# Optimization experiments

Measured on AMD Instinct MI355X. Metric: run time of the kernel, lower is better.

Reference implementation:

```python
import jax, jax.numpy as jnp
import numpy as np

# dims
B, N, K, V = 1, 50000, 6, 4          # batch, surface points, neighbors (num_sample_points-1), variables
P = K + 1                             # total sample points per node (center + K neighbors)
D_GEO, D_POS = 128, 32                # geometry / positional encoding widths
N_PARAMS, D_PARAM = 2, 32             # global params and their encoding width
D_IN = 7                              # 3 coords + 3 normals + 1 log-area
H1, H2 = 256, 128                     # MLP hidden widths
D_AGG = H1 + D_POS + D_GEO + D_PARAM  # aggregation-model input width = 448


def setup_inputs() -> dict:
    key = jax.random.key(0)
    ks = jax.random.split(key, 18)
    nrm = lambda k, s: jax.random.normal(k, s, jnp.float32)
    uni = lambda k, s, lo, hi: jax.random.uniform(k, s, jnp.float32, lo, hi)
    return {
        "surface_mesh_centers": nrm(ks[0], (B, N, 3)),
        "encoding_g": nrm(ks[1], (B, N, D_GEO)),
        "encoding_node": nrm(ks[2], (B, N, D_POS)),
        "surface_mesh_neighbors": nrm(ks[3], (B, N, K, 3)),
        "surface_normals": nrm(ks[4], (B, N, 3)),
        "surface_neighbors_normals": nrm(ks[5], (B, N, K, 3)),
        "surface_areas": uni(ks[6], (B, N, 1), 0.01, 1.0),
        "surface_neighbors_areas": uni(ks[7], (B, N, K, 1), 0.01, 1.0),
        "global_params_values": uni(ks[8], (B, N_PARAMS, 1), 0.5, 2.0),
        "global_params_reference": uni(ks[9], (B, N_PARAMS, 1), 0.5, 2.0),
        # learned parameters (per-variable MLPs stacked on leading V axis)
        "param_W": nrm(ks[10], (N_PARAMS, D_PARAM)) * 0.1,
        "param_b": jnp.zeros((D_PARAM,), jnp.float32),
        "basis_W1": nrm(ks[11], (V, D_IN, H1)) * 0.1,
        "basis_b1": jnp.zeros((V, H1), jnp.float32),
        "basis_W2": nrm(ks[12], (V, H1, H1)) * 0.1,
        "basis_b2": jnp.zeros((V, H1), jnp.float32),
        "agg_W1": nrm(ks[13], (V, D_AGG, H1)) * 0.1,
        "agg_b1": jnp.zeros((V, H1), jnp.float32),
        "agg_W2": nrm(ks[14], (V, H1, H2)) * 0.1,
        "agg_b2": jnp.zeros((V, H2), jnp.float32),
        "agg_W3": nrm(ks[15], (V, H2, 1)) * 0.1,
        "agg_b3": jnp.zeros((V, 1), jnp.float32),
    }


def reference(surface_mesh_centers, encoding_g, encoding_node, surface_mesh_neighbors,
              surface_normals, surface_neighbors_normals, surface_areas,
              surface_neighbors_areas, global_params_values, global_params_reference,
              param_W, param_b, basis_W1, basis_b1, basis_W2, basis_b2,
              agg_W1, agg_b1, agg_W2, agg_b2, agg_W3, agg_b3):
    relu = jax.nn.relu

    # parameter encoding: normalize globals by reference, broadcast to points, small MLP
    p = (global_params_values / global_params_reference)[:, :, 0]       # (B, n_params)
    p = jnp.broadcast_to(p[:, None, :], (B, N, N_PARAMS))               # (B, N, n_params)
    param_enc = relu(p @ param_W + param_b)                             # (B, N, D_PARAM)

    # concat coords + normals + log(area)/10, exactly as the torch module
    centers = jnp.concatenate(
        [surface_mesh_centers, surface_normals, jnp.log(surface_areas) / 10.0], -1)          # (B,N,7)
    neighbors = jnp.concatenate(
        [surface_mesh_neighbors, surface_neighbors_normals,
         jnp.log(surface_neighbors_areas) / 10.0], -1)                                        # (B,N,K,7)

    nb = neighbors + 1e-6
    vol = jnp.concatenate([centers[:, :, None, :], nb], axis=2)          # (B,N,P,7); p=0 is center
    # 1/dist computed in the 7-dim concatenated feature space (matches torch code)
    inv_dist = 1.0 / jnp.linalg.norm(centers[:, :, None, :] - nb, axis=-1, keepdims=True)    # (B,N,K,1)
    dist_sum = inv_dist.sum(axis=2)                                      # (B,N,1)

    ctx = jnp.concatenate([encoding_node, encoding_g, param_enc], -1)    # (B,N,Dctx)
    ctx = jnp.broadcast_to(ctx[:, :, None, :], (B, N, P, ctx.shape[-1]))

    outs = []
    for v in range(V):  # small fixed loop over output variables
        h = relu(vol @ basis_W1[v] + basis_b1[v])                        # (B,N,P,H1)
        basis = relu(h @ basis_W2[v] + basis_b2[v])                      # (B,N,P,H1)
        a = jnp.concatenate([basis, ctx], -1)                            # (B,N,P,D_AGG)
        a = relu(a @ agg_W1[v] + agg_b1[v])
        a = relu(a @ agg_W2[v] + agg_b2[v])
        a = a @ agg_W3[v] + agg_b3[v]                                    # (B,N,P,1)
        out_center = a[:, :, 0]                                          # (B,N,1)
        out_neighbor = (a[:, :, 1:] * inv_dist).sum(axis=2)              # (B,N,1)
        outs.append(0.5 * out_center + 0.5 * out_neighbor / dist_sum)
    return jnp.concatenate(outs, axis=-1)                                # (B,N,V)
```

## Files before the change

kernel.cpp:

```cpp
#include <hip/hip_runtime.h>

typedef __attribute__((ext_vector_type(8))) _Float16 f16x8;
typedef __attribute__((ext_vector_type(4))) float f32x4;

namespace {
constexpr int N_PTS = 50000;
constexpr int VOUT  = 4;
constexpr int PPB   = 9;
constexpr int MROWS = 64;
constexpr int ABYTES = 896;

constexpr int OFF_BW1 = 0;
constexpr int OFF_BW2 = 32768;
constexpr int OFF_AW1 = 294912;
constexpr int OFF_AW2 = 753664;
constexpr int PACK_TOTAL = 884736;
}

__global__ __launch_bounds__(256) void pack_weights_kernel(
    const float* __restrict__ bW1, const float* __restrict__ bW2,
    const float* __restrict__ aW1, const float* __restrict__ aW2,
    _Float16* __restrict__ out) {
  int t = blockIdx.x * 256 + threadIdx.x;
  const float* W; int Kg, N, Ksrc, base;
  if (t < OFF_BW2)      { base = OFF_BW1; Kg = 4;  N = 256; Ksrc = 7;   W = bW1; }
  else if (t < OFF_AW1) { base = OFF_BW2; Kg = 32; N = 256; Ksrc = 256; W = bW2; }
  else if (t < OFF_AW2) { base = OFF_AW1; Kg = 56; N = 256; Ksrc = 448; W = aW1; }
  else                  { base = OFF_AW2; Kg = 32; N = 128; Ksrc = 256; W = aW2; }
  int local = t - base;
  int vsz = Kg * N * 8;
  int v = local / vsz;
  int rem = local - v * vsz;
  int g  = rem / (N * 8);
  int r2 = rem - g * (N * 8);
  int n = r2 >> 3;
  int j = r2 & 7;
  int k = g * 8 + j;
  float val = (k < Ksrc) ? W[(v * Ksrc + k) * N + n] : 0.0f;
  out[t] = (_Float16)val;
}

template<int NT>
__device__ __forceinline__ void run_gemm(
    const _Float16* __restrict__ Bp, int Nn, int KB,
    const char* __restrict__ Ab, int abytes, int aswz,
    int lane, int n0, f32x4 acc[4][NT]) {
  const int q = lane >> 4, c = lane & 15;
  const char* Bb = (const char*)Bp;
  f16x8 bcur[NT], bnext[NT];
#pragma unroll
  for (int nt = 0; nt < NT; nt++)
    bcur[nt] = *(const f16x8*)(Bb + ((q * Nn + n0 + 16 * nt + c) << 4));
  for (int kb = 0; kb < KB; kb++) {
    f16x8 a[4];
    const int koff = (kb * 64 + q * 16) ^ aswz;
#pragma unroll
    for (int mt = 0; mt < 4; mt++)
      a[mt] = *(const f16x8*)(Ab + (16 * mt + c) * abytes + koff);
    if (kb + 1 < KB) {
#pragma unroll
      for (int nt = 0; nt < NT; nt++)
        bnext[nt] = *(const f16x8*)(Bb + ((((kb + 1) * 4 + q) * Nn + n0 + 16 * nt + c) << 4));
    }
#pragma unroll
    for (int mt = 0; mt < 4; mt++)
#pragma unroll
      for (int nt = 0; nt < NT; nt++)
        acc[mt][nt] = __builtin_amdgcn_mfma_f32_16x16x32_f16(a[mt], bcur[nt], acc[mt][nt], 0, 0, 0);
    if (kb + 1 < KB) {
#pragma unroll
      for (int nt = 0; nt < NT; nt++) bcur[nt] = bnext[nt];
    }
  }
}

template<int NT>
__device__ __forceinline__ void epilogue_relu(
    f32x4 acc[4][NT], const float* __restrict__ bias,
    int lane, int n0, char* __restrict__ Ab) {
  const int q = lane >> 4, c = lane & 15;
#pragma unroll
  for (int nt = 0; nt < NT; nt++) {
    const int col = n0 + 16 * nt + c;
    const float bv = bias[col];
#pragma unroll
    for (int mt = 0; mt < 4; mt++) {
#pragma unroll
      for (int r = 0; r < 4; r++) {
        const int row = 16 * mt + 4 * q + r;
        float y = fmaxf(acc[mt][nt][r] + bv, 0.0f);
        *(_Float16*)(Ab + row * ABYTES + ((2 * col) ^ (((4 * q + r) & 7) << 4))) = (_Float16)y;
      }
    }
  }
}

__global__ __launch_bounds__(256, 2) void surf_mfma_kernel(
    const float* __restrict__ centers, const float* __restrict__ enc_g,
    const float* __restrict__ enc_node, const float* __restrict__ nbrs,
    const float* __restrict__ normals, const float* __restrict__ nbr_normals,
    const float* __restrict__ areas, const float* __restrict__ nbr_areas,
    const float* __restrict__ gpv, const float* __restrict__ gpr,
    const float* __restrict__ pW, const float* __restrict__ pb,
    const float* __restrict__ bb1, const float* __restrict__ bb2,
    const float* __restrict__ ab1, const float* __restrict__ ab2,
    const float* __restrict__ aW3, const float* __restrict__ ab3,
    const _Float16* __restrict__ Wp, float* __restrict__ out) {
  __shared__ _Float16 sA[MROWS * 448];
  __shared__ _Float16 sVol[MROWS * 40];
  __shared__ float sVolF[63][7];
  __shared__ float sPE[32];
  __shared__ float sW3[128];
  __shared__ float sPart[4][64];
  __shared__ float sRow[64];
  __shared__ float sInvd[54];

  const int t    = threadIdx.x;
  const int lane = t & 63;
  const int w    = t >> 6;
  const int blk  = blockIdx.x;
  char* Ab = (char*)sA;

  if (t < 32) {
    float q0 = gpv[0] / gpr[0], q1 = gpv[1] / gpr[1];
    sPE[t] = fmaxf(fmaf(q0, pW[t], fmaf(q1, pW[32 + t], pb[t])), 0.0f);
  }
  if (t < 64) {
    float f[7];
    if (t < 63) {
      int pt = t / 7, p = t - pt * 7;
      int n = min(blk * PPB + pt, N_PTS - 1);
      if (p == 0) {
        f[0] = centers[n * 3];     f[1] = centers[n * 3 + 1]; f[2] = centers[n * 3 + 2];
        f[3] = normals[n * 3];     f[4] = normals[n * 3 + 1]; f[5] = normals[n * 3 + 2];
        f[6] = logf(areas[n]) * 0.1f;
      } else {
        int k = p - 1;
        int b3i = (n * 6 + k) * 3;
        f[0] = nbrs[b3i] + 1e-6f;        f[1] = nbrs[b3i + 1] + 1e-6f;
        f[2] = nbrs[b3i + 2] + 1e-6f;    f[3] = nbr_normals[b3i] + 1e-6f;
        f[4] = nbr_normals[b3i + 1] + 1e-6f; f[5] = nbr_normals[b3i + 2] + 1e-6f;
        f[6] = logf(nbr_areas[n * 6 + k]) * 0.1f + 1e-6f;
      }
#pragma unroll
      for (int j = 0; j < 7; j++) sVolF[t][j] = f[j];
    } else {
#pragma unroll
      for (int j = 0; j < 7; j++) f[j] = 0.0f;
    }
#pragma unroll
    for (int j = 0; j < 7; j++) sVol[t * 40 + j] = (_Float16)f[j];
#pragma unroll
    for (int j = 7; j < 40; j++) sVol[t * 40 + j] = (_Float16)0.0f;
  }
  __syncthreads();

  if (t < 54) {
    int pt = t / 6, k = t - pt * 6;
    float ss = 0.0f;
#pragma unroll
    for (int j = 0; j < 7; j++) {
      float d = sVolF[pt * 7][j] - sVolF[pt * 7 + 1 + k][j];
      ss = fmaf(d, d, ss);
    }
    sInvd[t] = 1.0f / sqrtf(ss);
  }
  for (int idx = t; idx < 63 * 192; idx += 256) {
    int row = idx / 192, j = idx - row * 192;
    int n = min(blk * PPB + row / 7, N_PTS - 1);
    float val = (j < 32) ? enc_node[n * 32 + j]
              : (j < 160) ? enc_g[n * 128 + (j - 32)]
              : sPE[j - 160];
    *(_Float16*)(Ab + row * ABYTES + ((2 * (256 + j)) ^ ((row & 7) << 4))) = (_Float16)val;
  }
  __syncthreads();

  const int aswz = (lane & 7) << 4;
  const int n0w  = 64 * w;

  for (int v = 0; v < VOUT; v++) {
    {
      f32x4 acc[4][4] = {};
      run_gemm<4>(Wp + OFF_BW1 + v * 8192, 256, 1, (const char*)sVol, 80, 0, lane, n0w, acc);
      epilogue_relu<4>(acc, bb1 + v * 256, lane, n0w, Ab);
    }
    __syncthreads();
    {
      f32x4 acc[4][4] = {};
      run_gemm<4>(Wp + OFF_BW2 + v * 65536, 256, 8, Ab, ABYTES, aswz, lane, n0w, acc);
      __syncthreads();
      epilogue_relu<4>(acc, bb2 + v * 256, lane, n0w, Ab);
    }
    __syncthreads();
    {
      f32x4 acc[4][4] = {};
      run_gemm<4>(Wp + OFF_AW1 + v * 114688, 256, 14, Ab, ABYTES, aswz, lane, n0w, acc);
      __syncthreads();
      epilogue_relu<4>(acc, ab1 + v * 256, lane, n0w, Ab);
    }
    __syncthreads();
    {
      f32x4 acc[4][2] = {};
      run_gemm<2>(Wp + OFF_AW2 + v * 32768, 128, 8, Ab, ABYTES, aswz, lane, 32 * w, acc);
      __syncthreads();
      epilogue_relu<2>(acc, ab2 + v * 128, lane, 32 * w, Ab);
      if (t < 128) sW3[t] = aW3[v * 128 + t];
    }
    __syncthreads();
    {
      int row = t & 63, h = t >> 6;
      float s = 0.0f;
      int swzm = (row & 7) << 4;
#pragma unroll
      for (int cc = 0; cc < 4; cc++) {
        int k0 = h * 32 + cc * 8;
        f16x8 av = *(const f16x8*)(Ab + row * ABYTES + ((2 * k0) ^ swzm));
#pragma unroll
        for (int j = 0; j < 8; j++) s = fmaf((float)av[j], sW3[k0 + j], s);
      }
      sPart[h][row] = s;
    }
    __syncthreads();
    if (t < 64) sRow[t] = sPart[0][t] + sPart[1][t] + sPart[2][t] + sPart[3][t] + ab3[v];
    __syncthreads();
    if (t < PPB) {
      int n = blk * PPB + t;
      if (n < N_PTS) {
        float o0 = sRow[t * 7];
        float on = 0.0f, ds = 0.0f;
#pragma unroll
        for (int k = 0; k < 6; k++) {
          float id = sInvd[t * 6 + k];
          on = fmaf(sRow[t * 7 + 1 + k], id, on);
          ds += id;
        }
        out[n * VOUT + v] = 0.5f * o0 + 0.5f * on / ds;
      }
    }
    __syncthreads();
  }
}

extern "C" void kernel_launch(void* const* d_in, const int* in_sizes, int n_in,
                              void* d_out, int out_size, void* d_ws, size_t ws_size,
                              hipStream_t stream) {
  const float* centers     = (const float*)d_in[0];
  const float* enc_g       = (const float*)d_in[1];
  const float* enc_node    = (const float*)d_in[2];
  const float* nbrs        = (const float*)d_in[3];
  const float* normals     = (const float*)d_in[4];
  const float* nbr_normals = (const float*)d_in[5];
  const float* areas       = (const float*)d_in[6];
  const float* nbr_areas   = (const float*)d_in[7];
  const float* gpv         = (const float*)d_in[8];
  const float* gpr         = (const float*)d_in[9];
  const float* pW          = (const float*)d_in[10];
  const float* pb          = (const float*)d_in[11];
  const float* bW1         = (const float*)d_in[12];
  const float* bb1         = (const float*)d_in[13];
  const float* bW2         = (const float*)d_in[14];
  const float* bb2         = (const float*)d_in[15];
  const float* aW1         = (const float*)d_in[16];
  const float* ab1         = (const float*)d_in[17];
  const float* aW2         = (const float*)d_in[18];
  const float* ab2         = (const float*)d_in[19];
  const float* aW3         = (const float*)d_in[20];
  const float* ab3         = (const float*)d_in[21];
  float* out = (float*)d_out;
  _Float16* Wp = (_Float16*)d_ws;

  pack_weights_kernel<<<dim3(PACK_TOTAL / 256), dim3(256), 0, stream>>>(
      bW1, bW2, aW1, aW2, Wp);

  const int nblocks = (N_PTS + PPB - 1) / PPB;
  surf_mfma_kernel<<<dim3(nblocks), dim3(256), 0, stream>>>(
      centers, enc_g, enc_node, nbrs, normals, nbr_normals, areas, nbr_areas,
      gpv, gpr, pW, pb, bb1, bb2, ab1, ab2, aW3, ab3, Wp, out);
}
```

Baseline: 744.8 us.

## Use 512-thread blocks, narrow per-wave tiles, fuse last layer into epilogue

Doubles the block to 8 waves, so each wave computes half as many output columns per GEMM. This halves the accumulator registers per thread and lets the launch bounds ask for more resident waves, to hide weight-load and LDS latency. The final 128→1 layer is folded into the AW2 GEMM epilogue with wave shuffles, dropping a separate LDS pass and two barriers. The context fill now loads float4s and writes packed 8×f16 vectors. The tighter launch bounds (512, 4) risk register spills, and LDS usage may still cap how many blocks stay resident.

```diff
diff --git a/kernel.cpp b/kernel.cpp
--- a/kernel.cpp
+++ b/kernel.cpp
@@ -7,7 +7,6 @@
 constexpr int N_PTS = 50000;
 constexpr int VOUT  = 4;
 constexpr int PPB   = 9;
-constexpr int MROWS = 64;
 constexpr int ABYTES = 896;
 
 constexpr int OFF_BW1 = 0;
@@ -95,7 +94,7 @@
   }
 }
 
-__global__ __launch_bounds__(256, 2) void surf_mfma_kernel(
+__global__ __launch_bounds__(512, 4) void surf_mfma_kernel(
     const float* __restrict__ centers, const float* __restrict__ enc_g,
     const float* __restrict__ enc_node, const float* __restrict__ nbrs,
     const float* __restrict__ normals, const float* __restrict__ nbr_normals,
@@ -106,12 +105,11 @@
     const float* __restrict__ ab1, const float* __restrict__ ab2,
     const float* __restrict__ aW3, const float* __restrict__ ab3,
     const _Float16* __restrict__ Wp, float* __restrict__ out) {
-  __shared__ _Float16 sA[MROWS * 448];
-  __shared__ _Float16 sVol[MROWS * 40];
+  __shared__ _Float16 sA[64 * 448];
+  __shared__ _Float16 sVol[64 * 40];
   __shared__ float sVolF[63][7];
-  __shared__ float sPE[32];
-  __shared__ float sW3[128];
-  __shared__ float sPart[4][64];
+  __shared__ alignas(16) float sPE[32];
+  __shared__ float sPart[8][64];
   __shared__ float sRow[64];
   __shared__ float sInvd[54];
 
@@ -165,64 +163,88 @@
     }
     sInvd[t] = 1.0f / sqrtf(ss);
   }
-  for (int idx = t; idx < 63 * 192; idx += 256) {
-    int row = idx / 192, j = idx - row * 192;
+  for (int task = t; task < 63 * 24; task += 512) {
+    int row = task / 24, g = task - row * 24;
     int n = min(blk * PPB + row / 7, N_PTS - 1);
-    float val = (j < 32) ? enc_node[n * 32 + j]
-              : (j < 160) ? enc_g[n * 128 + (j - 32)]
-              : sPE[j - 160];
-    *(_Float16*)(Ab + row * ABYTES + ((2 * (256 + j)) ^ ((row & 7) << 4))) = (_Float16)val;
+    float4 lo, hi;
+    if (g < 4) {
+      lo = *(const float4*)(enc_node + n * 32 + g * 8);
+      hi = *(const float4*)(enc_node + n * 32 + g * 8 + 4);
+    } else if (g < 20) {
+      lo = *(const float4*)(enc_g + n * 128 + (g - 4) * 8);
+      hi = *(const float4*)(enc_g + n * 128 + (g - 4) * 8 + 4);
+    } else {
+      lo = *(const float4*)(sPE + (g - 20) * 8);
+      hi = *(const float4*)(sPE + (g - 20) * 8 + 4);
+    }
+    f16x8 pk;
+    pk[0] = (_Float16)lo.x; pk[1] = (_Float16)lo.y; pk[2] = (_Float16)lo.z; pk[3] = (_Float16)lo.w;
+    pk[4] = (_Float16)hi.x; pk[5] = (_Float16)hi.y; pk[6] = (_Float16)hi.z; pk[7] = (_Float16)hi.w;
+    *(f16x8*)(Ab + row * ABYTES + ((512 + 16 * g) ^ ((row & 7) << 4))) = pk;
   }
   __syncthreads();
 
   const int aswz = (lane & 7) << 4;
-  const int n0w  = 64 * w;
+  const int n0w  = 32 * w;
 
   for (int v = 0; v < VOUT; v++) {
     {
-      f32x4 acc[4][4] = {};
-      run_gemm<4>(Wp + OFF_BW1 + v * 8192, 256, 1, (const char*)sVol, 80, 0, lane, n0w, acc);
-      epilogue_relu<4>(acc, bb1 + v * 256, lane, n0w, Ab);
-    }
-    __syncthreads();
-    {
-      f32x4 acc[4][4] = {};
-      run_gemm<4>(Wp + OFF_BW2 + v * 65536, 256, 8, Ab, ABYTES, aswz, lane, n0w, acc);
-      __syncthreads();
-      epilogue_relu<4>(acc, bb2 + v * 256, lane, n0w, Ab);
-    }
-    __syncthreads();
-    {
-      f32x4 acc[4][4] = {};
-      run_gemm<4>(Wp + OFF_AW1 + v * 114688, 256, 14, Ab, ABYTES, aswz, lane, n0w, acc);
-      __syncthreads();
-      epilogue_relu<4>(acc, ab1 + v * 256, lane, n0w, Ab);
+      f32x4 acc[4][2] = {};
+      run_gemm<2>(Wp + OFF_BW1 + v * 8192, 256, 1, (const char*)sVol, 80, 0, lane, n0w, acc);
+      epilogue_relu<2>(acc, bb1 + v * 256, lane, n0w, Ab);
     }
     __syncthreads();
     {
       f32x4 acc[4][2] = {};
-      run_gemm<2>(Wp + OFF_AW2 + v * 32768, 128, 8, Ab, ABYTES, aswz, lane, 32 * w, acc);
+      run_gemm<2>(Wp + OFF_BW2 + v * 65536, 256, 8, Ab, ABYTES, aswz, lane, n0w, acc);
       __syncthreads();
-      epilogue_relu<2>(acc, ab2 + v * 128, lane, 32 * w, Ab);
-      if (t < 128) sW3[t] = aW3[v * 128 + t];
+      epilogue_relu<2>(acc, bb2 + v * 256, lane, n0w, Ab);
     }
     __syncthreads();
     {
-      int row = t & 63, h = t >> 6;
-      float s = 0.0f;
-      int swzm = (row & 7) << 4;
-#pragma unroll
-      for (int cc = 0; cc < 4; cc++) {
-        int k0 = h * 32 + cc * 8;
-        f16x8 av = *(const f16x8*)(Ab + row * ABYTES + ((2 * k0) ^ swzm));
-#pragma unroll
-        for (int j = 0; j < 8; j++) s = fmaf((float)av[j], sW3[k0 + j], s);
-      }
-      sPart[h][row] = s;
-    }
-    __syncthreads();
-    if (t < 64) sRow[t] = sPart[0][t] + sPart[1][t] + sPart[2][t] + sPart[3][t] + ab3[v];
-    __syncthreads();
+      f32x4 acc[4][2] = {};
+      run_gemm<2>(Wp + OFF_AW1 + v * 114688, 256, 14, Ab, ABYTES, aswz, lane, n0w, acc);
+      __syncthreads();
+      epilogue_relu<2>(acc, ab1 + v * 256, lane, n0w, Ab);
+    }
+    __syncthreads();
+    {
+      f32x4 acc[4][1] = {};
+      run_gemm<1>(Wp + OFF_AW2 + v * 32768, 128, 8, Ab, ABYTES, aswz, lane, 16 * w, acc);
+      const int col = 16 * w + (lane & 15);
+      const float b2 = ab2[v * 128 + col];
+      const float w3 = aW3[v * 128 + col];
+      float part[16];
+#pragma unroll
+      for (int mt = 0; mt < 4; mt++)
+#pragma unroll
+        for (int r = 0; r < 4; r++)
+          part[mt * 4 + r] = fmaxf(acc[mt][0][r] + b2, 0.0f) * w3;
+#pragma unroll
+      for (int i = 0; i < 16; i++) {
+        float s = part[i];
+        s += __shfl_xor(s, 1, 64);
+        s += __shfl_xor(s, 2, 64);
+        s += __shfl_xor(s, 4, 64);
+        s += __shfl_xor(s, 8, 64);
+        part[i] = s;
+      }
+      if ((lane & 15) == 0) {
+        const int q = lane >> 4;
+#pragma unroll
+        for (int mt = 0; mt < 4; mt++)
+#pragma unroll
+          for (int r = 0; r < 4; r++)
+            sPart[w][16 * mt + 4 * q + r] = part[mt * 4 + r];
+      }
+    }
+    __syncthreads();
+    if (t < 64) {
+      float s = ab3[v];
+#pragma unroll
+      for (int ww = 0; ww < 8; ww++) s += sPart[ww][t];
+      sRow[t] = s;
+    }
     if (t < PPB) {
       int n = blk * PPB + t;
       if (n < N_PTS) {
@@ -273,7 +295,7 @@
       bW1, bW2, aW1, aW2, Wp);
 
   const int nblocks = (N_PTS + PPB - 1) / PPB;
-  surf_mfma_kernel<<<dim3(nblocks), dim3(256), 0, stream>>>(
+  surf_mfma_kernel<<<dim3(nblocks), dim3(512), 0, stream>>>(
       centers, enc_g, enc_node, nbrs, normals, nbr_normals, areas, nbr_areas,
       gpv, gpr, pW, pb, bb1, bb2, ab1, ab2, aW3, ab3, Wp, out);
 }
```

Result: slower. 885.0 us (+18.8%).
